# Kernel tuning notes

Hardware: AMD Instinct MI355X
Metric: run time of the kernel (lower is better)

Reference implementation:

```python
import jax, jax.numpy as jnp
import numpy as np

B, H, T, D = 2, 16, 2048, 64
R1, R2 = 4, 8


def setup_inputs() -> dict:
    key = jax.random.key(0)
    ks = jax.random.split(key, 7)
    return {
        "q": jax.random.normal(ks[0], (B, H, T, D), dtype=jnp.float32),
        "k": jax.random.normal(ks[1], (B, H, T, D), dtype=jnp.float32),
        "v": jax.random.normal(ks[2], (B, H, T, D), dtype=jnp.float32),
        "W_q": jax.random.normal(ks[3], (H, D, R1 * R2), dtype=jnp.float32) / np.sqrt(D),
        "W_k": jax.random.normal(ks[4], (H, D, R1 * R2), dtype=jnp.float32) / np.sqrt(D),
        "core1": jax.random.normal(ks[5], (H, R1), dtype=jnp.float32),
        "core2": jax.random.normal(ks[6], (H, R2), dtype=jnp.float32),
    }


def reference(q, k, v, W_q, W_k, core1, core2):
    """Kronecker low-rank (LSR) causal attention.

    scores[b,h,m,n] = (1/sqrt(R1*R2)) * sum_r kron[h,r] * (q@W_q)[b,h,m,r] * (k@W_k)[b,h,n,r]
    where kron[h] = core1[h] (x) core2[h]  (per-head Kronecker product).
    """
    Hh, r1 = core1.shape
    r2 = core2.shape[1]
    # per-head Kronecker core vector: (H, R1*R2)
    kron = (core1[:, :, None] * core2[:, None, :]).reshape(Hh, r1 * r2)
    scale = 1.0 / jnp.sqrt(jnp.float32(r1 * r2))
    # low-rank projections, rank R = R1*R2
    q_lr = jnp.einsum("bhtd,hdr->bhtr", q, W_q) * kron[None, :, None, :]  # [B,H,T,R]
    k_lr = jnp.einsum("bhtd,hdr->bhtr", k, W_k)                            # [B,H,T,R]
    scores = jnp.einsum("bhmr,bhnr->bhmn", q_lr, k_lr) * scale             # [B,H,T,T]
    t = q.shape[2]
    causal = jnp.tril(jnp.ones((t, t), dtype=bool))
    scores = jnp.where(causal[None, None], scores, -jnp.inf)
    p = jax.nn.softmax(scores, axis=-1)
    return jnp.einsum("bhmn,bhnd->bhmd", p, v)
```

## Files before the change

kernel.cpp:

```cpp
#include <hip/hip_runtime.h>

typedef _Float16 f16;
typedef _Float16 f16x2 __attribute__((ext_vector_type(2)));
typedef _Float16 f16x8 __attribute__((ext_vector_type(8)));
typedef float    f32x4 __attribute__((ext_vector_type(4)));
typedef float    f32x16 __attribute__((ext_vector_type(16)));
typedef unsigned int u32;

constexpr int B_ = 2, H_ = 16, T_ = 2048, D_ = 64, R_ = 32, NT = 32;
constexpr int MT = 16;
constexpr int NROW = B_ * H_ * T_;

__device__ __forceinline__ f32x4 mfma16(f16x8 a, f16x8 b, f32x4 c) {
  return __builtin_amdgcn_mfma_f32_16x16x32_f16(a, b, c, 0, 0, 0);
}
__device__ __forceinline__ f32x16 mfma32(f16x8 a, f16x8 b, f32x16 c) {
  return __builtin_amdgcn_mfma_f32_32x32x16_f16(a, b, c, 0, 0, 0);
}
__device__ __forceinline__ u32 pkrtz(float a, float b) {
  return __builtin_bit_cast(u32, __builtin_amdgcn_cvt_pkrtz(a, b));
}


__global__ __launch_bounds__(256) void proj_kernel(
    const float* __restrict__ q, const float* __restrict__ k, const float* __restrict__ v,
    const float* __restrict__ Wq, const float* __restrict__ Wk,
    const float* __restrict__ c1, const float* __restrict__ c2,
    f16* __restrict__ qlr, f16* __restrict__ klr, f16* __restrict__ vt)
{
  __shared__ f16   sv[64 * 65];
  __shared__ float sW[2][64 * 33];
  __shared__ f16   sO[2][64 * 40];

  const int tid = threadIdx.x, w = tid >> 6, lane = tid & 63;
  const int l15 = lane & 15, l4 = lane >> 4;
  const int bh = blockIdx.x >> 5, h = bh & (H_ - 1);
  const int jt = blockIdx.x & 31, t0 = jt * 64;

  const float* vb = v + ((size_t)bh * T_ + t0) * D_;
  float4 vld[4];
#pragma unroll
  for (int it = 0; it < 4; ++it) vld[it] = ((const float4*)vb)[it * 256 + tid];

  const int m = t0 + 16 * w + l15;
  const float* qr = q + ((size_t)bh * T_ + m) * D_;
  const float* kr = k + ((size_t)bh * T_ + m) * D_;
  f16x8 aq[2], ak[2];
#pragma unroll
  for (int kc = 0; kc < 2; ++kc) {
    float4 x0 = *(const float4*)(qr + kc * 32 + 8 * l4);
    float4 x1 = *(const float4*)(qr + kc * 32 + 8 * l4 + 4);
    float4 y0 = *(const float4*)(kr + kc * 32 + 8 * l4);
    float4 y1 = *(const float4*)(kr + kc * 32 + 8 * l4 + 4);
    f16x8 A, K;
    A[0]=(f16)x0.x; A[1]=(f16)x0.y; A[2]=(f16)x0.z; A[3]=(f16)x0.w;
    A[4]=(f16)x1.x; A[5]=(f16)x1.y; A[6]=(f16)x1.z; A[7]=(f16)x1.w;
    K[0]=(f16)y0.x; K[1]=(f16)y0.y; K[2]=(f16)y0.z; K[3]=(f16)y0.w;
    K[4]=(f16)y1.x; K[5]=(f16)y1.y; K[6]=(f16)y1.z; K[7]=(f16)y1.w;
    aq[kc] = A; ak[kc] = K;
  }
  const float* Wqh = Wq + (size_t)h * D_ * R_;
  const float* Wkh = Wk + (size_t)h * D_ * R_;
  float4 wq0 = ((const float4*)Wqh)[tid * 2], wq1 = ((const float4*)Wqh)[tid * 2 + 1];
  float4 wk0 = ((const float4*)Wkh)[tid * 2], wk1 = ((const float4*)Wkh)[tid * 2 + 1];

#pragma unroll
  for (int it = 0; it < 4; ++it) {
    const int i4 = it * 256 + tid, t = i4 >> 4, dq = (i4 & 15) * 4;
    sv[t * 65 + dq    ] = (f16)vld[it].x;
    sv[t * 65 + dq + 1] = (f16)vld[it].y;
    sv[t * 65 + dq + 2] = (f16)vld[it].z;
    sv[t * 65 + dq + 3] = (f16)vld[it].w;
  }
  {
    const int d = tid >> 2, r0 = (tid & 3) * 8;
    float* pq = &sW[0][d * 33 + r0];
    float* pk = &sW[1][d * 33 + r0];
    pq[0]=wq0.x; pq[1]=wq0.y; pq[2]=wq0.z; pq[3]=wq0.w;
    pq[4]=wq1.x; pq[5]=wq1.y; pq[6]=wq1.z; pq[7]=wq1.w;
    pk[0]=wk0.x; pk[1]=wk0.y; pk[2]=wk0.z; pk[3]=wk0.w;
    pk[4]=wk1.x; pk[5]=wk1.y; pk[6]=wk1.z; pk[7]=wk1.w;
  }
  __syncthreads();

  const f32x4 z4 = {0.f, 0.f, 0.f, 0.f};
#pragma unroll
  for (int nt = 0; nt < 2; ++nt) {
    const int r = 16 * nt + l15;
    f16x8 bq[2], bk[2];
#pragma unroll
    for (int kc = 0; kc < 2; ++kc)
#pragma unroll
      for (int j2 = 0; j2 < 8; ++j2) {
        const int d = kc * 32 + 8 * l4 + j2;
        bq[kc][j2] = (f16)sW[0][d * 33 + r];
        bk[kc][j2] = (f16)sW[1][d * 33 + r];
      }
    f32x4 accq = mfma16(aq[0], bq[0], z4); accq = mfma16(aq[1], bq[1], accq);
    f32x4 acck = mfma16(ak[0], bk[0], z4); acck = mfma16(ak[1], bk[1], acck);
    const float scl = c1[h * 4 + (r >> 3)] * c2[h * 8 + (r & 7)] *
                      (0.17677669529663687f * 1.4426950408889634f);
#pragma unroll
    for (int i = 0; i < 4; ++i) {
      const int row = 16 * w + 4 * l4 + i;
      sO[0][row * 40 + r] = (f16)(accq[i] * scl);
      sO[1][row * 40 + r] = (f16)acck[i];
    }
  }
  __syncthreads();

  {
    const int row = tid >> 2, q4 = tid & 3;
    const size_t base = ((((size_t)bh * 32 + jt) * 2 + (q4 >> 1)) * 2 + (q4 & 1)) * 64 + row;
    *(f16x8*)(qlr + base * 8) = *(const f16x8*)&sO[0][row * 40 + q4 * 8];
    *(f16x8*)(klr + base * 8) = *(const f16x8*)&sO[1][row * 40 + q4 * 8];
  }
#pragma unroll
  for (int it = 0; it < 8; ++it) {
    const int d = tid >> 2, i2 = (tid & 3) * 2, t = it * 8 + i2;
    f16x2 pr; pr[0] = sv[t * 65 + d]; pr[1] = sv[(t + 1) * 65 + d];
    *(f16x2*)(vt + (((size_t)bh * 32 + jt) * 8 + it) * 512 + d * 8 + i2) = pr;
  }
}

__global__ __launch_bounds__(256, 4) void attn_kernel(
    const f16* __restrict__ qlr, const f16* __restrict__ klr,
    const f16* __restrict__ vt, f16* __restrict__ On, float2* __restrict__ ml,
    const int ns_shift)
{
  const int tid = threadIdx.x, w = tid >> 6, lane = tid & 63;
  const int l31 = lane & 31, hh = lane >> 5;
  const int NS = 1 << ns_shift;
  const int bh = blockIdx.x & 31;
  const int rest = blockIdx.x >> 5;
  const int mt = (MT - 1) - (rest >> ns_shift);
  const int s  = rest & (NS - 1);
  const int mw = mt * 128 + 32 * w;

  const int jm = mw >> 6, mloc = (mw & 63) + l31;
  const f16* qb = qlr + (((size_t)bh * 32 + jm) * 2048) + hh * 512 + (size_t)mloc * 8;
  const f16x8 bq0 = *(const f16x8*)(qb);
  const f16x8 bq1 = *(const f16x8*)(qb + 1024);

  const f16* kb = klr + (size_t)bh * 32 * 2048;
  const f16* vb = vt + (size_t)bh * 32 * 4096;

  f32x16 oacc[2];
  f32x16 z16;
#pragma unroll
  for (int e = 0; e < 16; ++e) { z16[e] = 0.f; oacc[0][e] = 0.f; oacc[1][e] = 0.f; }
  float mi = -1e30f, li = 0.f;

  const int jw = 2 * mt + (w >> 1);
  for (int j = s; j <= jw; j += NS) {
    const f16* kj = kb + (size_t)j * 2048;
    const f16* vj = vb + (size_t)j * 4096;

    f32x16 sc[2];
#pragma unroll
    for (int nt = 0; nt < 2; ++nt) {
      const int nl = 32 * nt + l31;
      const f16x8 a0 = *(const f16x8*)(kj + hh * 512 + nl * 8);
      const f16x8 a1 = *(const f16x8*)(kj + 1024 + hh * 512 + nl * 8);
      sc[nt] = mfma32(a0, bq0, z16);
      sc[nt] = mfma32(a1, bq1, sc[nt]);
    }
    const int n0 = j * 64;
    if (n0 + 63 > mw) {
      const int lim = mw + l31 - n0;
#pragma unroll
      for (int nt = 0; nt < 2; ++nt)
#pragma unroll
        for (int e = 0; e < 16; ++e) {
          const int nv = 32 * nt + 4 * hh + (e & 3) + 8 * (e >> 2);
          if (nv > lim) sc[nt][e] = -1e30f;
        }
    }

    float rm = -1e30f;
#pragma unroll
    for (int nt = 0; nt < 2; ++nt)
#pragma unroll
      for (int e = 0; e < 16; ++e) rm = fmaxf(rm, sc[nt][e]);
    rm = fmaxf(rm, __shfl_xor(rm, 32));
    const float mn = fmaxf(mi, rm);
    const float alpha = exp2f(mi - mn);
    float rs = 0.f;
    u32 pk[2][8];
#pragma unroll
    for (int nt = 0; nt < 2; ++nt)
#pragma unroll
      for (int s4 = 0; s4 < 4; ++s4) {
        const float p0 = exp2f(sc[nt][4 * s4 + 0] - mn);
        const float p1 = exp2f(sc[nt][4 * s4 + 1] - mn);
        const float p2 = exp2f(sc[nt][4 * s4 + 2] - mn);
        const float p3 = exp2f(sc[nt][4 * s4 + 3] - mn);
        rs += (p0 + p1) + (p2 + p3);
        pk[nt][2 * s4]     = pkrtz(p0, p1);
        pk[nt][2 * s4 + 1] = pkrtz(p2, p3);
      }
    rs += __shfl_xor(rs, 32);
    li = li * alpha + rs; mi = mn;
#pragma unroll
    for (int c = 0; c < 2; ++c)
#pragma unroll
      for (int e = 0; e < 16; ++e) oacc[c][e] *= alpha;

#pragma unroll
    for (int nt = 0; nt < 2; ++nt)
#pragma unroll
      for (int kcp = 0; kcp < 2; ++kcp) {
        const int kc = 2 * nt + kcp;
        const u32 sA = hh ? pk[nt][4 * kcp]     : pk[nt][4 * kcp + 2];
        const u32 sB = hh ? pk[nt][4 * kcp + 1] : pk[nt][4 * kcp + 3];
        const u32 kA = hh ? pk[nt][4 * kcp + 2] : pk[nt][4 * kcp];
        const u32 kB = hh ? pk[nt][4 * kcp + 3] : pk[nt][4 * kcp + 1];
        const u32 r0 = (u32)__shfl_xor((int)sA, 32);
        const u32 r1 = (u32)__shfl_xor((int)sB, 32);
        union { f16x8 v; u32 u[4]; } bp;
        bp.u[0] = hh ? r0 : kA;
        bp.u[1] = hh ? r1 : kB;
        bp.u[2] = hh ? kA : r0;
        bp.u[3] = hh ? kB : r1;
#pragma unroll
        for (int c = 0; c < 2; ++c) {
          const f16x8 av = *(const f16x8*)(vj + (size_t)(kc * 2 + hh) * 512 + (32 * c + l31) * 8);
          oacc[c] = mfma32(av, bp.v, oacc[c]);
        }
      }
  }

  const float invl = li > 0.f ? 1.f / li : 0.f;
  f16* ob = On + (((size_t)s * 32 + bh) * T_ + mw + l31) * D_;
#pragma unroll
  for (int c = 0; c < 2; ++c)
#pragma unroll
    for (int s4 = 0; s4 < 4; ++s4) {
      const int d0 = 32 * c + 8 * s4 + 4 * hh;
      const u32 e0 = pkrtz(oacc[c][4 * s4] * invl, oacc[c][4 * s4 + 1] * invl);
      const u32 e1 = pkrtz(oacc[c][4 * s4 + 2] * invl, oacc[c][4 * s4 + 3] * invl);
      *(u32*)(ob + d0)     = e0;
      *(u32*)(ob + d0 + 2) = e1;
    }
  if (!hh) {
    float2 mlv; mlv.x = mi; mlv.y = li;
    ml[((size_t)s * 32 + bh) * T_ + mw + l31] = mlv;
  }
}

__global__ __launch_bounds__(256) void merge_kernel(
    const f16* __restrict__ On, const float2* __restrict__ ml,
    float* __restrict__ out, const int NS)
{
  const int row = blockIdx.x * 32 + (threadIdx.x >> 3);
  const int d0 = (threadIdx.x & 7) * 8;
  float res[8];
  if (NS == 1) {
    const f16x8 o0 = *(const f16x8*)(On + (size_t)row * 64 + d0);
#pragma unroll
    for (int e = 0; e < 8; ++e) res[e] = (float)o0[e];
  } else {
    float2 mls[4];
    float ms = -3e38f;
    for (int s = 0; s < NS; ++s) {
      mls[s] = ml[(size_t)s * NROW + row];
      ms = fmaxf(ms, mls[s].x);
    }
    float wt[4], wsum = 0.f;
    for (int s = 0; s < NS; ++s) {
      wt[s] = exp2f(mls[s].x - ms) * mls[s].y;
      wsum += wt[s];
    }
    const float inv = 1.f / wsum;
#pragma unroll
    for (int e = 0; e < 8; ++e) res[e] = 0.f;
    for (int s = 0; s < NS; ++s) {
      const f16x8 o = *(const f16x8*)(On + ((size_t)s * NROW + row) * 64 + d0);
      const float c = wt[s] * inv;
#pragma unroll
      for (int e = 0; e < 8; ++e) res[e] += c * (float)o[e];
    }
  }
  float* ob = out + (size_t)row * 64 + d0;
  f32x4 r0, r1;
#pragma unroll
  for (int e = 0; e < 4; ++e) { r0[e] = res[e]; r1[e] = res[4 + e]; }
  *(f32x4*)ob = r0;
  *(f32x4*)(ob + 4) = r1;
}

extern "C" void kernel_launch(void* const* d_in, const int* in_sizes, int n_in,
                              void* d_out, int out_size, void* d_ws, size_t ws_size,
                              hipStream_t stream) {
  const float* q  = (const float*)d_in[0];
  const float* k  = (const float*)d_in[1];
  const float* v  = (const float*)d_in[2];
  const float* Wq = (const float*)d_in[3];
  const float* Wk = (const float*)d_in[4];
  const float* c1 = (const float*)d_in[5];
  const float* c2 = (const float*)d_in[6];
  float* out = (float*)d_out;

  f16* qlr = (f16*)d_ws;
  f16* klr = qlr + (size_t)B_ * H_ * T_ * R_;
  f16* vt  = klr + (size_t)B_ * H_ * T_ * R_;
  f16* On  = vt + (size_t)B_ * H_ * T_ * D_;

  const size_t projB = (size_t)16 * 1024 * 1024;
  const size_t perSplit = (size_t)NROW * D_ * 2 + (size_t)NROW * 8;
  int ns_shift = 0;
  if (ws_size >= projB + 2 * perSplit) ns_shift = 1;
  const int NS = 1 << ns_shift;
  float2* ml = (float2*)(On + (size_t)NS * NROW * D_);

  proj_kernel<<<B_ * H_ * NT, 256, 0, stream>>>(q, k, v, Wq, Wk, c1, c2, qlr, klr, vt);
  attn_kernel<<<B_ * H_ * MT * NS, 256, 0, stream>>>(qlr, klr, vt, On, ml, ns_shift);
  merge_kernel<<<NROW / 32, 256, 0, stream>>>(On, ml, out, NS);
}
```

Baseline: 165.4 us.

## Split KV across wave pairs inside block and merge in shared memory

Attention blocks now own a 64-row query tile; two pairs of waves each handle half the key tiles (even or odd) for the same 32 query rows. The partial outputs and softmax stats are combined through LDS in-block and written directly as fp32, so the separate merge kernel and the fp16 global partial buffers go away. Grid becomes 1024 blocks instead of 512 or 1024 split blocks. This adds about 35KB of LDS per block, which may limit occupancy against the launch bound of 4 blocks, plus a block-wide barrier.

```diff
diff --git a/kernel.cpp b/kernel.cpp
--- a/kernel.cpp
+++ b/kernel.cpp
@@ -8,8 +8,6 @@
 typedef unsigned int u32;
 
 constexpr int B_ = 2, H_ = 16, T_ = 2048, D_ = 64, R_ = 32, NT = 32;
-constexpr int MT = 16;
-constexpr int NROW = B_ * H_ * T_;
 
 __device__ __forceinline__ f32x4 mfma16(f16x8 a, f16x8 b, f32x4 c) {
   return __builtin_amdgcn_mfma_f32_16x16x32_f16(a, b, c, 0, 0, 0);
@@ -125,20 +123,21 @@
 
 __global__ __launch_bounds__(256, 4) void attn_kernel(
     const f16* __restrict__ qlr, const f16* __restrict__ klr,
-    const f16* __restrict__ vt, f16* __restrict__ On, float2* __restrict__ ml,
-    const int ns_shift)
+    const f16* __restrict__ vt, float* __restrict__ out)
 {
+  __shared__ __align__(16) float  s_o[4][32 * 68];
+  __shared__ float2 s_ml[4][32];
+
   const int tid = threadIdx.x, w = tid >> 6, lane = tid & 63;
   const int l31 = lane & 31, hh = lane >> 5;
-  const int NS = 1 << ns_shift;
+  const int p = w & 1, hw = w >> 1;
   const int bh = blockIdx.x & 31;
-  const int rest = blockIdx.x >> 5;
-  const int mt = (MT - 1) - (rest >> ns_shift);
-  const int s  = rest & (NS - 1);
-  const int mw = mt * 128 + 32 * w;
-
-  const int jm = mw >> 6, mloc = (mw & 63) + l31;
-  const f16* qb = qlr + (((size_t)bh * 32 + jm) * 2048) + hh * 512 + (size_t)mloc * 8;
+  const int qt = 31 - (blockIdx.x >> 5);
+  const int m0 = qt * 64;
+  const int mw = m0 + 32 * hw;
+
+  const int mloc = 32 * hw + l31;
+  const f16* qb = qlr + (((size_t)bh * 32 + qt) * 2048) + hh * 512 + (size_t)mloc * 8;
   const f16x8 bq0 = *(const f16x8*)(qb);
   const f16x8 bq1 = *(const f16x8*)(qb + 1024);
 
@@ -151,8 +150,7 @@
   for (int e = 0; e < 16; ++e) { z16[e] = 0.f; oacc[0][e] = 0.f; oacc[1][e] = 0.f; }
   float mi = -1e30f, li = 0.f;
 
-  const int jw = 2 * mt + (w >> 1);
-  for (int j = s; j <= jw; j += NS) {
+  for (int j = p; j <= qt; j += 2) {
     const f16* kj = kb + (size_t)j * 2048;
     const f16* vj = vb + (size_t)j * 4096;
 
@@ -230,63 +228,41 @@
       }
   }
 
-  const float invl = li > 0.f ? 1.f / li : 0.f;
-  f16* ob = On + (((size_t)s * 32 + bh) * T_ + mw + l31) * D_;
 #pragma unroll
   for (int c = 0; c < 2; ++c)
 #pragma unroll
     for (int s4 = 0; s4 < 4; ++s4) {
-      const int d0 = 32 * c + 8 * s4 + 4 * hh;
-      const u32 e0 = pkrtz(oacc[c][4 * s4] * invl, oacc[c][4 * s4 + 1] * invl);
-      const u32 e1 = pkrtz(oacc[c][4 * s4 + 2] * invl, oacc[c][4 * s4 + 3] * invl);
-      *(u32*)(ob + d0)     = e0;
-      *(u32*)(ob + d0 + 2) = e1;
+      f32x4 ov;
+#pragma unroll
+      for (int e = 0; e < 4; ++e) ov[e] = oacc[c][4 * s4 + e];
+      *(f32x4*)&s_o[w][l31 * 68 + 32 * c + 8 * s4 + 4 * hh] = ov;
     }
   if (!hh) {
     float2 mlv; mlv.x = mi; mlv.y = li;
-    ml[((size_t)s * 32 + bh) * T_ + mw + l31] = mlv;
-  }
-}
-
-__global__ __launch_bounds__(256) void merge_kernel(
-    const f16* __restrict__ On, const float2* __restrict__ ml,
-    float* __restrict__ out, const int NS)
-{
-  const int row = blockIdx.x * 32 + (threadIdx.x >> 3);
-  const int d0 = (threadIdx.x & 7) * 8;
-  float res[8];
-  if (NS == 1) {
-    const f16x8 o0 = *(const f16x8*)(On + (size_t)row * 64 + d0);
-#pragma unroll
-    for (int e = 0; e < 8; ++e) res[e] = (float)o0[e];
-  } else {
-    float2 mls[4];
-    float ms = -3e38f;
-    for (int s = 0; s < NS; ++s) {
-      mls[s] = ml[(size_t)s * NROW + row];
-      ms = fmaxf(ms, mls[s].x);
-    }
-    float wt[4], wsum = 0.f;
-    for (int s = 0; s < NS; ++s) {
-      wt[s] = exp2f(mls[s].x - ms) * mls[s].y;
-      wsum += wt[s];
-    }
-    const float inv = 1.f / wsum;
-#pragma unroll
-    for (int e = 0; e < 8; ++e) res[e] = 0.f;
-    for (int s = 0; s < NS; ++s) {
-      const f16x8 o = *(const f16x8*)(On + ((size_t)s * NROW + row) * 64 + d0);
-      const float c = wt[s] * inv;
-#pragma unroll
-      for (int e = 0; e < 8; ++e) res[e] += c * (float)o[e];
-    }
-  }
-  float* ob = out + (size_t)row * 64 + d0;
-  f32x4 r0, r1;
-#pragma unroll
-  for (int e = 0; e < 4; ++e) { r0[e] = res[e]; r1[e] = res[4 + e]; }
-  *(f32x4*)ob = r0;
-  *(f32x4*)(ob + 4) = r1;
+    s_ml[w][l31] = mlv;
+  }
+  __syncthreads();
+
+  {
+    const int mrow = tid >> 2;
+    const int d0 = (tid & 3) * 16;
+    const int wA = (mrow >> 5) * 2, wB = wA + 1, ml = mrow & 31;
+    const float2 a = s_ml[wA][ml], b = s_ml[wB][ml];
+    const float ms = fmaxf(a.x, b.x);
+    const float eA = exp2f(a.x - ms), eB = exp2f(b.x - ms);
+    const float inv = 1.f / (eA * a.y + eB * b.y);
+    const float cA = eA * inv, cB = eB * inv;
+    float* ob = out + ((size_t)bh * T_ + m0 + mrow) * D_ + d0;
+#pragma unroll
+    for (int seg = 0; seg < 4; ++seg) {
+      const f32x4 oA = *(const f32x4*)&s_o[wA][ml * 68 + d0 + 4 * seg];
+      const f32x4 oB = *(const f32x4*)&s_o[wB][ml * 68 + d0 + 4 * seg];
+      f32x4 r;
+#pragma unroll
+      for (int e = 0; e < 4; ++e) r[e] = cA * oA[e] + cB * oB[e];
+      *(f32x4*)(ob + 4 * seg) = r;
+    }
+  }
 }
 
 extern "C" void kernel_launch(void* const* d_in, const int* in_sizes, int n_in,
@@ -304,16 +280,7 @@
   f16* qlr = (f16*)d_ws;
   f16* klr = qlr + (size_t)B_ * H_ * T_ * R_;
   f16* vt  = klr + (size_t)B_ * H_ * T_ * R_;
-  f16* On  = vt + (size_t)B_ * H_ * T_ * D_;
-
-  const size_t projB = (size_t)16 * 1024 * 1024;
-  const size_t perSplit = (size_t)NROW * D_ * 2 + (size_t)NROW * 8;
-  int ns_shift = 0;
-  if (ws_size >= projB + 2 * perSplit) ns_shift = 1;
-  const int NS = 1 << ns_shift;
-  float2* ml = (float2*)(On + (size_t)NS * NROW * D_);
 
   proj_kernel<<<B_ * H_ * NT, 256, 0, stream>>>(q, k, v, Wq, Wk, c1, c2, qlr, klr, vt);
-  attn_kernel<<<B_ * H_ * MT * NS, 256, 0, stream>>>(qlr, klr, vt, On, ml, ns_shift);
-  merge_kernel<<<NROW / 32, 256, 0, stream>>>(On, ml, out, NS);
-}
+  attn_kernel<<<B_ * H_ * NT, 256, 0, stream>>>(qlr, klr, vt, out);
+}
```

After: 157.0 us. -5.1%, faster.
